# Kernel tuning notes

Measured on AMD Instinct MI355X. Metric: run time of the kernel, lower is better.

The kernel has to match this reference:

```python
import jax, jax.numpy as jnp
import numpy as np

HEAD_NUM = 8
HEAD_DIM = 32
EPS = 0.0  # torch.linalg.norm division has no eps; keep exact


def setup_inputs() -> dict:
    key = jax.random.key(0)
    k1, k2 = jax.random.split(key)
    batch_s = jax.random.normal(k1, (2048, HEAD_NUM * HEAD_DIM), dtype=jnp.float32)
    batch_ro = jax.random.normal(k2, (8192, HEAD_NUM * HEAD_DIM), dtype=jnp.float32)
    return {"batch_s": batch_s, "batch_ro": batch_ro}


def reference(batch_s, batch_ro):
    N, M = batch_s.shape[0], batch_ro.shape[0]
    s = batch_s.reshape(N, HEAD_NUM, HEAD_DIM)   # [N, H, D]
    ro = batch_ro.reshape(M, HEAD_NUM, HEAD_DIM)  # [M, H, D]
    # L2-normalize each head vector
    s = s / jnp.linalg.norm(s, axis=-1, keepdims=True)
    ro = ro / jnp.linalg.norm(ro, axis=-1, keepdims=True)
    # per-head cosine similarity: [N, M, H]
    dist = jnp.einsum('nhd,mhd->nmh', s, ro)
    # max-pool over heads -> [N, M]
    return jnp.max(dist, axis=-1)
```

## Files before the change

### kernel.cpp

```cpp
#include <hip/hip_runtime.h>

#define S_ROWS 2048
#define RO_ROWS 8192
#define HEADS 8
#define HDIM 32
#define ROWLEN 256
#define NB_S (S_ROWS / 16)
#define NB_RO (RO_ROWS / 16)

typedef __attribute__((ext_vector_type(8))) short bf16x8;
typedef __attribute__((ext_vector_type(4))) float f32x4;
typedef __attribute__((ext_vector_type(4))) short s16x4;

__device__ __forceinline__ short f32_to_bf16_rne(float f) {
    union { float f; unsigned u; } v; v.f = f;
    return (short)((v.u + 0x7fffu + ((v.u >> 16) & 1u)) >> 16);
}

__global__ __launch_bounds__(256) void mhd_normalize(const float* __restrict__ s,
                                                     const float* __restrict__ ro,
                                                     short* __restrict__ sF,
                                                     short* __restrict__ roF) {
    const int v   = blockIdx.x * 256 + threadIdx.x;
    const int dg  = v & 7;
    const int r16 = (v >> 3) & 15;
    const int u   = v >> 7;
    const int h   = u & 7;
    const int nb_all = u >> 3;
    const bool isS = nb_all < NB_S;
    const int nb  = isS ? nb_all : nb_all - NB_S;
    const int n   = nb * 16 + r16;

    const float* src = isS ? s : ro;
    f32x4 x = *(const f32x4*)(src + (size_t)n * ROWLEN + h * HDIM + dg * 4);
    float ss = x[0] * x[0] + x[1] * x[1] + x[2] * x[2] + x[3] * x[3];
    ss += __shfl_xor(ss, 1);
    ss += __shfl_xor(ss, 2);
    ss += __shfl_xor(ss, 4);
    const float inv = rsqrtf(ss);
    s16x4 r;
    r[0] = f32_to_bf16_rne(x[0] * inv);
    r[1] = f32_to_bf16_rne(x[1] * inv);
    r[2] = f32_to_bf16_rne(x[2] * inv);
    r[3] = f32_to_bf16_rne(x[3] * inv);

    short* dst = isS ? sF : roF;
    const int NB = isS ? NB_S : NB_RO;
    *(s16x4*)(dst + ((size_t)(h * NB + nb) * 16 + r16) * 32 + dg * 4) = r;
}

__global__ __launch_bounds__(256) void mhd_dist(const short* __restrict__ sF,
                                                const short* __restrict__ roF,
                                                float* __restrict__ out) {
    __shared__ float lds[4][16][68];
    const int lane = threadIdx.x & 63;
    const int wave = threadIdx.x >> 6;
    const int wr = wave >> 1;
    const int wc = wave & 1;
    const int bid = blockIdx.x;
    const int swz = (bid & 7) * 128 + (bid >> 3);
    const int tile_r = swz >> 6;
    const int tile_c = swz & 63;
    const int l15 = lane & 15;
    const int kg = lane >> 4;

    const int nbA = tile_r * 8 + wr * 4;
    const int nbB = tile_c * 8 + wc * 4;
    const size_t laneOff = (size_t)l15 * 32 + kg * 8;

    bf16x8 B[HEADS][4];
#pragma unroll
    for (int h = 0; h < HEADS; ++h)
#pragma unroll
        for (int j = 0; j < 4; ++j)
            B[h][j] = *(const bf16x8*)(roF + (size_t)(h * NB_RO + nbB + j) * 512 + laneOff);

    float* outBase = out + (size_t)(tile_r * 128 + wr * 64) * RO_ROWS
                         + tile_c * 128 + wc * 64;
    const int srow = lane >> 4;
    const int scol = (lane & 15) * 4;

#pragma unroll
    for (int i = 0; i < 4; ++i) {
        f32x4 runmax[4];
#pragma unroll
        for (int j = 0; j < 4; ++j)
            runmax[j] = (f32x4){-3.0e38f, -3.0e38f, -3.0e38f, -3.0e38f};

#pragma unroll
        for (int h = 0; h < HEADS; ++h) {
            const bf16x8 a = *(const bf16x8*)(sF + (size_t)(h * NB_S + nbA + i) * 512 + laneOff);
#pragma unroll
            for (int j = 0; j < 4; ++j) {
                f32x4 acc = {0.f, 0.f, 0.f, 0.f};
                acc = __builtin_amdgcn_mfma_f32_16x16x32_bf16(B[h][j], a, acc, 0, 0, 0);
#pragma unroll
                for (int q = 0; q < 4; ++q)
                    runmax[j][q] = fmaxf(runmax[j][q], acc[q]);
            }
        }

#pragma unroll
        for (int j = 0; j < 4; ++j)
            *(f32x4*)&lds[wave][l15][kg * 4 + j * 16] = runmax[j];
#pragma unroll
        for (int t = 0; t < 4; ++t) {
            const int rowL = t * 4 + srow;
            f32x4 vv = *(const f32x4*)&lds[wave][rowL][scol];
            *(f32x4*)(outBase + (size_t)(i * 16 + rowL) * RO_ROWS + scol) = vv;
        }
    }
}

extern "C" void kernel_launch(void* const* d_in, const int* in_sizes, int n_in,
                              void* d_out, int out_size, void* d_ws, size_t ws_size,
                              hipStream_t stream) {
    const float* batch_s  = (const float*)d_in[0];
    const float* batch_ro = (const float*)d_in[1];
    float* out = (float*)d_out;

    short* sF  = (short*)d_ws;
    short* roF = sF + (size_t)S_ROWS * ROWLEN;

    const int totalV4 = (S_ROWS + RO_ROWS) * ROWLEN / 4;
    mhd_normalize<<<totalV4 / 256, 256, 0, stream>>>(batch_s, batch_ro, sF, roF);

    mhd_dist<<<(S_ROWS / 128) * (RO_ROWS / 128), 256, 0, stream>>>(sF, roF, out);
}
```

Measured before the change: 102.6 us.

## Shrink dist tile to 128x64 and loop heads outermost with small register footprint

Each block now covers 128 s-rows by 64 ro-rows, with each wave owning 32 full-width rows instead of a 64x64 quadrant. The head loop moves outermost, loading only 2 A and 4 B fragments per head and keeping a 2x4 running-max array, instead of preloading all 32 B fragments per head up front. The launch grid doubles and the block-index swizzle is dropped. The aim is lower register pressure and higher occupancy to hide load latency, at the cost of more redundant global fragment loads and possibly worse L2 locality without the swizzle.

```diff
diff --git a/kernel.cpp b/kernel.cpp
--- a/kernel.cpp
+++ b/kernel.cpp
@@ -55,54 +55,54 @@
     __shared__ float lds[4][16][68];
     const int lane = threadIdx.x & 63;
     const int wave = threadIdx.x >> 6;
-    const int wr = wave >> 1;
-    const int wc = wave & 1;
-    const int bid = blockIdx.x;
-    const int swz = (bid & 7) * 128 + (bid >> 3);
-    const int tile_r = swz >> 6;
-    const int tile_c = swz & 63;
+    const int tile_r = blockIdx.x >> 7;
+    const int tile_c = blockIdx.x & 127;
     const int l15 = lane & 15;
     const int kg = lane >> 4;
 
-    const int nbA = tile_r * 8 + wr * 4;
-    const int nbB = tile_c * 8 + wc * 4;
+    const int nbA = tile_r * 8 + wave * 2;
+    const int nbB = tile_c * 4;
     const size_t laneOff = (size_t)l15 * 32 + kg * 8;
 
-    bf16x8 B[HEADS][4];
+    f32x4 runmax[2][4];
 #pragma unroll
-    for (int h = 0; h < HEADS; ++h)
+    for (int i = 0; i < 2; ++i)
 #pragma unroll
         for (int j = 0; j < 4; ++j)
-            B[h][j] = *(const bf16x8*)(roF + (size_t)(h * NB_RO + nbB + j) * 512 + laneOff);
+            runmax[i][j] = (f32x4){-3.0e38f, -3.0e38f, -3.0e38f, -3.0e38f};
 
-    float* outBase = out + (size_t)(tile_r * 128 + wr * 64) * RO_ROWS
-                         + tile_c * 128 + wc * 64;
-    const int srow = lane >> 4;
-    const int scol = (lane & 15) * 4;
-
+#pragma unroll 2
+    for (int h = 0; h < HEADS; ++h) {
+        const short* aBase = sF  + (size_t)(h * NB_S  + nbA) * 512 + laneOff;
+        const short* bBase = roF + (size_t)(h * NB_RO + nbB) * 512 + laneOff;
+        bf16x8 a[2], b[4];
 #pragma unroll
-    for (int i = 0; i < 4; ++i) {
-        f32x4 runmax[4];
+        for (int i = 0; i < 2; ++i)
+            a[i] = *(const bf16x8*)(aBase + (size_t)i * 512);
 #pragma unroll
         for (int j = 0; j < 4; ++j)
-            runmax[j] = (f32x4){-3.0e38f, -3.0e38f, -3.0e38f, -3.0e38f};
-
+            b[j] = *(const bf16x8*)(bBase + (size_t)j * 512);
 #pragma unroll
-        for (int h = 0; h < HEADS; ++h) {
-            const bf16x8 a = *(const bf16x8*)(sF + (size_t)(h * NB_S + nbA + i) * 512 + laneOff);
+        for (int i = 0; i < 2; ++i)
 #pragma unroll
             for (int j = 0; j < 4; ++j) {
                 f32x4 acc = {0.f, 0.f, 0.f, 0.f};
-                acc = __builtin_amdgcn_mfma_f32_16x16x32_bf16(B[h][j], a, acc, 0, 0, 0);
+                acc = __builtin_amdgcn_mfma_f32_16x16x32_bf16(b[j], a[i], acc, 0, 0, 0);
 #pragma unroll
                 for (int q = 0; q < 4; ++q)
-                    runmax[j][q] = fmaxf(runmax[j][q], acc[q]);
+                    runmax[i][j][q] = fmaxf(runmax[i][j][q], acc[q]);
             }
-        }
+    }
 
+    float* outBase = out + (size_t)(tile_r * 128 + wave * 32) * RO_ROWS
+                         + tile_c * 64;
+    const int srow = lane >> 4;
+    const int scol = (lane & 15) * 4;
+#pragma unroll
+    for (int i = 0; i < 2; ++i) {
 #pragma unroll
         for (int j = 0; j < 4; ++j)
-            *(f32x4*)&lds[wave][l15][kg * 4 + j * 16] = runmax[j];
+            *(f32x4*)&lds[wave][l15][kg * 4 + j * 16] = runmax[i][j];
 #pragma unroll
         for (int t = 0; t < 4; ++t) {
             const int rowL = t * 4 + srow;
@@ -125,5 +125,5 @@
     const int totalV4 = (S_ROWS + RO_ROWS) * ROWLEN / 4;
     mhd_normalize<<<totalV4 / 256, 256, 0, stream>>>(batch_s, batch_ro, sF, roF);
 
-    mhd_dist<<<(S_ROWS / 128) * (RO_ROWS / 128), 256, 0, stream>>>(sF, roF, out);
+    mhd_dist<<<(S_ROWS / 128) * (RO_ROWS / 64), 256, 0, stream>>>(sF, roF, out);
 }
```

After: 102.9 us. About the same (+0.3%).

## Stage head fragments through double-buffered LDS with direct global-to-LDS loads

Applied to the files above, without the earlier changes.

The normalize kernel now writes fragments in MFMA lane order, so each 16x32 fragment is one contiguous 1 KB block. The distance kernel now uses 512-thread blocks covering a 256x128 tile. Per head it stages A and B fragments into a double-buffered LDS area via global_load_lds, prefetching the next head while MFMAs run on the current one. This replaces per-wave register-resident B across all heads with shared LDS reuse across waves and keeps all 16 running-max accumulators live. It adds a barrier per head and more register pressure, and it drops the block swizzle used for L2 locality.

```diff
diff --git a/kernel.cpp b/kernel.cpp
--- a/kernel.cpp
+++ b/kernel.cpp
@@ -15,6 +15,12 @@
 __device__ __forceinline__ short f32_to_bf16_rne(float f) {
     union { float f; unsigned u; } v; v.f = f;
     return (short)((v.u + 0x7fffu + ((v.u >> 16) & 1u)) >> 16);
+}
+
+__device__ __forceinline__ void gll16(const void* g, void* l) {
+    __builtin_amdgcn_global_load_lds(
+        (const __attribute__((address_space(1))) unsigned*)g,
+        (__attribute__((address_space(3))) unsigned*)l, 16, 0, 0);
 }
 
 __global__ __launch_bounds__(256) void mhd_normalize(const float* __restrict__ s,
@@ -46,67 +52,95 @@
 
     short* dst = isS ? sF : roF;
     const int NB = isS ? NB_S : NB_RO;
-    *(s16x4*)(dst + ((size_t)(h * NB + nb) * 16 + r16) * 32 + dg * 4) = r;
+    const int lane_in_frag = ((dg >> 1) << 4) + r16;
+    const size_t off = ((size_t)(h * NB + nb) << 9) + lane_in_frag * 8 + (dg & 1) * 4;
+    *(s16x4*)(dst + off) = r;
 }
 
-__global__ __launch_bounds__(256) void mhd_dist(const short* __restrict__ sF,
-                                                const short* __restrict__ roF,
-                                                float* __restrict__ out) {
-    __shared__ float lds[4][16][68];
+__global__ __launch_bounds__(512, 4) void mhd_dist(const short* __restrict__ sF,
+                                                   const short* __restrict__ roF,
+                                                   float* __restrict__ out) {
+    __shared__ short lds[2][24 * 512];
     const int lane = threadIdx.x & 63;
     const int wave = threadIdx.x >> 6;
     const int wr = wave >> 1;
     const int wc = wave & 1;
-    const int bid = blockIdx.x;
-    const int swz = (bid & 7) * 128 + (bid >> 3);
-    const int tile_r = swz >> 6;
-    const int tile_c = swz & 63;
+    const int tile_r = blockIdx.x >> 6;
+    const int tile_c = blockIdx.x & 63;
+    const int nbA0 = tile_r * 16;
+    const int nbB0 = tile_c * 8;
+
+    const short* gsrc[3];
+    size_t hstep[3];
+#pragma unroll
+    for (int t = 0; t < 3; ++t) {
+        const int f = wave * 3 + t;
+        if (f < 16) {
+            gsrc[t] = sF + ((size_t)(nbA0 + f) << 9) + lane * 8;
+            hstep[t] = (size_t)NB_S << 9;
+        } else {
+            gsrc[t] = roF + ((size_t)(nbB0 + (f - 16)) << 9) + lane * 8;
+            hstep[t] = (size_t)NB_RO << 9;
+        }
+    }
+
+    f32x4 rmax[4][4];
+#pragma unroll
+    for (int i = 0; i < 4; ++i)
+#pragma unroll
+        for (int j = 0; j < 4; ++j)
+            rmax[i][j] = (f32x4){-3.0e38f, -3.0e38f, -3.0e38f, -3.0e38f};
+
+#pragma unroll
+    for (int t = 0; t < 3; ++t)
+        gll16(gsrc[t], &lds[0][(wave * 3 + t) * 512]);
+    __syncthreads();
+
+#pragma unroll 1
+    for (int h = 0; h < HEADS; ++h) {
+        const int buf = h & 1;
+        if (h < HEADS - 1) {
+#pragma unroll
+            for (int t = 0; t < 3; ++t)
+                gll16(gsrc[t] + (size_t)(h + 1) * hstep[t],
+                      &lds[buf ^ 1][(wave * 3 + t) * 512]);
+        }
+        bf16x8 a[4], b[4];
+#pragma unroll
+        for (int i = 0; i < 4; ++i)
+            a[i] = *(const bf16x8*)&lds[buf][(wr * 4 + i) * 512 + lane * 8];
+#pragma unroll
+        for (int j = 0; j < 4; ++j)
+            b[j] = *(const bf16x8*)&lds[buf][(16 + wc * 4 + j) * 512 + lane * 8];
+#pragma unroll
+        for (int i = 0; i < 4; ++i)
+#pragma unroll
+            for (int j = 0; j < 4; ++j) {
+                f32x4 acc = {0.f, 0.f, 0.f, 0.f};
+                acc = __builtin_amdgcn_mfma_f32_16x16x32_bf16(b[j], a[i], acc, 0, 0, 0);
+#pragma unroll
+                for (int q = 0; q < 4; ++q)
+                    rmax[i][j][q] = fmaxf(rmax[i][j][q], acc[q]);
+            }
+        __syncthreads();
+    }
+
+    float* eld = (float*)&lds[0][0] + wave * 16 * 68;
     const int l15 = lane & 15;
     const int kg = lane >> 4;
-
-    const int nbA = tile_r * 8 + wr * 4;
-    const int nbB = tile_c * 8 + wc * 4;
-    const size_t laneOff = (size_t)l15 * 32 + kg * 8;
-
-    bf16x8 B[HEADS][4];
-#pragma unroll
-    for (int h = 0; h < HEADS; ++h)
-#pragma unroll
-        for (int j = 0; j < 4; ++j)
-            B[h][j] = *(const bf16x8*)(roF + (size_t)(h * NB_RO + nbB + j) * 512 + laneOff);
-
-    float* outBase = out + (size_t)(tile_r * 128 + wr * 64) * RO_ROWS
+    float* outBase = out + (size_t)(tile_r * 256 + wr * 64) * RO_ROWS
                          + tile_c * 128 + wc * 64;
     const int srow = lane >> 4;
     const int scol = (lane & 15) * 4;
-
 #pragma unroll
     for (int i = 0; i < 4; ++i) {
-        f32x4 runmax[4];
 #pragma unroll
         for (int j = 0; j < 4; ++j)
-            runmax[j] = (f32x4){-3.0e38f, -3.0e38f, -3.0e38f, -3.0e38f};
-
-#pragma unroll
-        for (int h = 0; h < HEADS; ++h) {
-            const bf16x8 a = *(const bf16x8*)(sF + (size_t)(h * NB_S + nbA + i) * 512 + laneOff);
-#pragma unroll
-            for (int j = 0; j < 4; ++j) {
-                f32x4 acc = {0.f, 0.f, 0.f, 0.f};
-                acc = __builtin_amdgcn_mfma_f32_16x16x32_bf16(B[h][j], a, acc, 0, 0, 0);
-#pragma unroll
-                for (int q = 0; q < 4; ++q)
-                    runmax[j][q] = fmaxf(runmax[j][q], acc[q]);
-            }
-        }
-
-#pragma unroll
-        for (int j = 0; j < 4; ++j)
-            *(f32x4*)&lds[wave][l15][kg * 4 + j * 16] = runmax[j];
+            *(f32x4*)&eld[l15 * 68 + kg * 4 + j * 16] = rmax[i][j];
 #pragma unroll
         for (int t = 0; t < 4; ++t) {
             const int rowL = t * 4 + srow;
-            f32x4 vv = *(const f32x4*)&lds[wave][rowL][scol];
+            f32x4 vv = *(const f32x4*)&eld[rowL * 68 + scol];
             *(f32x4*)(outBase + (size_t)(i * 16 + rowL) * RO_ROWS + scol) = vv;
         }
     }
@@ -125,5 +159,5 @@
     const int totalV4 = (S_ROWS + RO_ROWS) * ROWLEN / 4;
     mhd_normalize<<<totalV4 / 256, 256, 0, stream>>>(batch_s, batch_ro, sF, roF);
 
-    mhd_dist<<<(S_ROWS / 128) * (RO_ROWS / 128), 256, 0, stream>>>(sF, roF, out);
+    mhd_dist<<<(S_ROWS / 256) * (RO_ROWS / 128), 512, 0, stream>>>(sF, roF, out);
 }
```

After: 97.61 us. 4.9% less time.

## Restructure dist kernel: lane-contiguous fragment layout, head-outer loop, XCD-mapped 256x128 tiles

Applied to the files above, without the earlier changes.

The normalize kernel now writes bf16 fragments in per-lane MFMA order, so each lane reads a contiguous 16-byte chunk. The dist kernel uses 512-thread blocks covering 256x128 output tiles, with the block-to-row mapping chosen by XCD. The loop now runs heads on the outside and keeps a 4x4 grid of running-max accumulators in registers instead of preloading all B fragments for every head. The aim is to cut register pressure, improve load coalescing and L2 locality per XCD, and raise occupancy. In exchange it adds more live accumulators and keeps only a small number of loads in flight per head iteration.

```diff
diff --git a/kernel.cpp b/kernel.cpp
--- a/kernel.cpp
+++ b/kernel.cpp
@@ -46,67 +46,69 @@
 
     short* dst = isS ? sF : roF;
     const int NB = isS ? NB_S : NB_RO;
-    *(s16x4*)(dst + ((size_t)(h * NB + nb) * 16 + r16) * 32 + dg * 4) = r;
+    const int lane_in_frag = ((dg >> 1) << 4) + r16;
+    const size_t off = ((size_t)(h * NB + nb) << 9) + lane_in_frag * 8 + (dg & 1) * 4;
+    *(s16x4*)(dst + off) = r;
 }
 
-__global__ __launch_bounds__(256) void mhd_dist(const short* __restrict__ sF,
-                                                const short* __restrict__ roF,
-                                                float* __restrict__ out) {
-    __shared__ float lds[4][16][68];
+__global__ __launch_bounds__(512, 4) void mhd_dist(const short* __restrict__ sF,
+                                                   const short* __restrict__ roF,
+                                                   float* __restrict__ out) {
+    __shared__ float elds[8][16][68];
     const int lane = threadIdx.x & 63;
     const int wave = threadIdx.x >> 6;
     const int wr = wave >> 1;
     const int wc = wave & 1;
-    const int bid = blockIdx.x;
-    const int swz = (bid & 7) * 128 + (bid >> 3);
-    const int tile_r = swz >> 6;
-    const int tile_c = swz & 63;
-    const int l15 = lane & 15;
-    const int kg = lane >> 4;
+    const int xcd = blockIdx.x & 7;
+    const int q   = blockIdx.x >> 3;
+    const int nbA = xcd * 16 + wr * 4;
+    const int nbB = q * 8 + wc * 4;
+    const size_t laneOff = (size_t)lane * 8;
 
-    const int nbA = tile_r * 8 + wr * 4;
-    const int nbB = tile_c * 8 + wc * 4;
-    const size_t laneOff = (size_t)l15 * 32 + kg * 8;
-
-    bf16x8 B[HEADS][4];
+    f32x4 rmax[4][4];
 #pragma unroll
-    for (int h = 0; h < HEADS; ++h)
+    for (int i = 0; i < 4; ++i)
 #pragma unroll
         for (int j = 0; j < 4; ++j)
-            B[h][j] = *(const bf16x8*)(roF + (size_t)(h * NB_RO + nbB + j) * 512 + laneOff);
+            rmax[i][j] = (f32x4){-3.0e38f, -3.0e38f, -3.0e38f, -3.0e38f};
 
-    float* outBase = out + (size_t)(tile_r * 128 + wr * 64) * RO_ROWS
-                         + tile_c * 128 + wc * 64;
-    const int srow = lane >> 4;
-    const int scol = (lane & 15) * 4;
-
+#pragma unroll 1
+    for (int h = 0; h < HEADS; ++h) {
+        const short* aBase = sF  + ((size_t)(h * NB_S  + nbA) << 9) + laneOff;
+        const short* bBase = roF + ((size_t)(h * NB_RO + nbB) << 9) + laneOff;
+        bf16x8 a[4], b[4];
 #pragma unroll
-    for (int i = 0; i < 4; ++i) {
-        f32x4 runmax[4];
+        for (int i = 0; i < 4; ++i) {
+            a[i] = *(const bf16x8*)(aBase + ((size_t)i << 9));
+            b[i] = *(const bf16x8*)(bBase + ((size_t)i << 9));
+        }
 #pragma unroll
-        for (int j = 0; j < 4; ++j)
-            runmax[j] = (f32x4){-3.0e38f, -3.0e38f, -3.0e38f, -3.0e38f};
-
-#pragma unroll
-        for (int h = 0; h < HEADS; ++h) {
-            const bf16x8 a = *(const bf16x8*)(sF + (size_t)(h * NB_S + nbA + i) * 512 + laneOff);
+        for (int i = 0; i < 4; ++i)
 #pragma unroll
             for (int j = 0; j < 4; ++j) {
                 f32x4 acc = {0.f, 0.f, 0.f, 0.f};
-                acc = __builtin_amdgcn_mfma_f32_16x16x32_bf16(B[h][j], a, acc, 0, 0, 0);
+                acc = __builtin_amdgcn_mfma_f32_16x16x32_bf16(b[j], a[i], acc, 0, 0, 0);
 #pragma unroll
-                for (int q = 0; q < 4; ++q)
-                    runmax[j][q] = fmaxf(runmax[j][q], acc[q]);
+                for (int q2 = 0; q2 < 4; ++q2)
+                    rmax[i][j][q2] = fmaxf(rmax[i][j][q2], acc[q2]);
             }
-        }
+    }
 
+    const int l15 = lane & 15;
+    const int kg = lane >> 4;
+    float* outBase = out + (size_t)(xcd * 256 + wr * 64) * RO_ROWS
+                         + q * 128 + wc * 64;
+    const int srow = lane >> 4;
+    const int scol = (lane & 15) * 4;
+#pragma unroll
+    for (int i = 0; i < 4; ++i) {
 #pragma unroll
         for (int j = 0; j < 4; ++j)
-            *(f32x4*)&lds[wave][l15][kg * 4 + j * 16] = runmax[j];
+            *(f32x4*)&elds[wave][l15][kg * 4 + j * 16] = rmax[i][j];
 #pragma unroll
         for (int t = 0; t < 4; ++t) {
             const int rowL = t * 4 + srow;
-            f32x4 vv = *(const f32x4*)&lds[wave][rowL][scol];
+            f32x4 vv = *(const f32x4*)&elds[wave][rowL][scol];
             *(f32x4*)(outBase + (size_t)(i * 16 + rowL) * RO_ROWS + scol) = vv;
         }
     }
@@ -125,5 +127,5 @@
     const int totalV4 = (S_ROWS + RO_ROWS) * ROWLEN / 4;
     mhd_normalize<<<totalV4 / 256, 256, 0, stream>>>(batch_s, batch_ro, sF, roF);
 
-    mhd_dist<<<(S_ROWS / 128) * (RO_ROWS / 128), 256, 0, stream>>>(sF, roF, out);
+    mhd_dist<<<(S_ROWS / 256) * (RO_ROWS / 128), 512, 0, stream>>>(sF, roF, out);
 }
```

New measurement: 95.94 us. 6.5% less time.
